# Kernel tuning notes

Measured on AMD Instinct MI355X. Metric: run time of the kernel, lower is better.

The kernel has to match this reference:

```python
import jax, jax.numpy as jnp
import numpy as np


def setup_inputs() -> dict:
    key = jax.random.key(0)
    ks = jax.random.split(key, 6)
    B, H, N, C, O, G = 4, 24, 512, 120, 512, 5
    x = jax.random.normal(ks[0], (B, H, N, C), dtype=jnp.float32)
    t_indices = jnp.arange(H, dtype=jnp.int64)
    time_emb = jax.random.normal(ks[1], (H, 8), dtype=jnp.float32)
    # kaiming-uniform-ish init for base linear weight
    fan_in = C + 8
    bound = float(np.sqrt(6.0 / fan_in))
    base_w = jax.random.uniform(ks[2], (O, C + 8), minval=-bound, maxval=bound, dtype=jnp.float32)
    base_b = jax.random.uniform(ks[3], (O,), minval=-1.0 / np.sqrt(fan_in), maxval=1.0 / np.sqrt(fan_in), dtype=jnp.float32)
    spline_weight = jax.random.uniform(ks[4], (O, C + 8, G), minval=-0.1, maxval=0.1, dtype=jnp.float32)
    return {"x": x, "t_indices": t_indices, "time_emb": time_emb,
            "base_w": base_w, "base_b": base_b, "spline_weight": spline_weight}


def reference(x, t_indices, time_emb, base_w, base_b, spline_weight):
    B, H, N, C = x.shape
    G = spline_weight.shape[-1]
    grid = jnp.linspace(-1.0, 1.0, G, dtype=x.dtype)  # non-trainable buffer
    # time embedding lookup, broadcast over batch and nodes: [B,H,N,8]
    t_emb = jnp.broadcast_to(time_emb[t_indices][None, :, None, :], (B, H, N, time_emb.shape[-1]))
    x_in = jnp.concatenate([x, t_emb], axis=-1)  # [B,H,N,C+8]
    # base path: SiLU then linear
    base = jnp.einsum('bhni,oi->bhno', jax.nn.silu(x_in), base_w) + base_b
    # RBF basis: [B,H,N,C+8,G]
    inv_h = (G - 1) / 2.0  # 1 / (2/(G-1))
    basis = jnp.exp(-(((x_in[..., None] - grid) * inv_h) ** 2))
    spline = jnp.einsum('bhnig,oig->bhno', basis, spline_weight)
    return base + spline
```

## Files before the change

kernel.cpp:

```cpp
#include <hip/hip_runtime.h>
#include <hip/hip_bf16.h>

typedef __attribute__((ext_vector_type(4))) float f32x4;
typedef __attribute__((ext_vector_type(8))) short bf16x8;

#define GLDS16(gp, lp) __builtin_amdgcn_global_load_lds( \
    (__attribute__((address_space(1))) void*)(void*)(gp), \
    (__attribute__((address_space(3))) void*)(lp), 16, 0, 0)

static constexpr int Mtot = 49152;
static constexpr int Otot = 512;
static constexpr int Hh   = 24;

__device__ inline unsigned short f2bf(float f) {
    __hip_bfloat16 h = __float2bfloat16(f);
    unsigned short u;
    __builtin_memcpy(&u, &h, 2);
    return u;
}

__global__ __launch_bounds__(256) void prep_W(
        const float* __restrict__ bw, const float* __restrict__ sw,
        uint4* __restrict__ Wt)
{
    const int tid = blockIdx.x * 256 + threadIdx.x;
    const int col = tid & 511;
    const int cc  = tid >> 9;
    const int k0  = cc * 8;
    unsigned short s[8];
    #pragma unroll
    for (int e = 0; e < 8; ++e) {
        const int k = k0 + e;
        const int i = k / 6, f = k - i * 6;
        const float v = (f == 0) ? bw[col * 128 + i]
                                 : sw[(col * 128 + i) * 5 + (f - 1)];
        s[e] = f2bf(v);
    }
    uint4 u;
    u.x = s[0] | ((unsigned)s[1] << 16);
    u.y = s[2] | ((unsigned)s[3] << 16);
    u.z = s[4] | ((unsigned)s[5] << 16);
    u.w = s[6] | ((unsigned)s[7] << 16);
    Wt[tid] = u;
}

__global__ __launch_bounds__(256, 3) void gemm_kan(
        const float* __restrict__ x, const int* __restrict__ t_idx,
        const float* __restrict__ temb,
        const char* __restrict__ Wt,
        const float* __restrict__ bias,
        float* __restrict__ out)
{
    __shared__ char Alds[12 * 128 * 16];
    __shared__ char Blds[12 * 128 * 16];
    const int t    = threadIdx.x;
    const int wave = t >> 6;
    const int lane = t & 63;
    const int ll   = lane & 15;
    const int q4   = lane >> 4;
    const int wm   = (wave >> 1) * 64;
    const int wn   = (wave & 1) * 64;

    const int bid = blockIdx.x;
    const int swz = (bid & 7) * 192 + (bid >> 3);
    const int m_base = (swz >> 2) * 128;
    const int n_base = (swz & 3) * 128;

    const int row = t >> 1;
    const int hh  = t & 1;
    const int ht  = t_idx[(m_base >> 9) % Hh];
    const float* xrow = x + (size_t)(m_base + row) * 120;
    const float* trow = temb + ht * 8;

    auto chanptr = [&](int i0) -> const float* {
        return (i0 < 120) ? (xrow + i0) : (trow + (i0 - 120));
    };

    f32x4 acc[4][4] = {};

    float4 xa, xb;
    {
        const float* p = chanptr(hh * 8);
        xa = *(const float4*)p;
        xb = *(const float4*)(p + 4);
    }

    constexpr float C1 = 0.36787944117f;
    constexpr float C4 = 0.01831563889f;

    #pragma unroll
    for (int it = 0; it < 8; ++it) {
        #pragma unroll
        for (int j = 0; j < 6; ++j) {
            const int c = wave * 3 + (j >> 1);
            const int g = (j & 1) * 64;
            const char* src = Wt + (((size_t)(it * 12 + c) * 512 + n_base + g) << 4)
                              + lane * 16;
            GLDS16(src, Blds + ((c * 128 + g) << 4));
        }

        const float4 ca = xa, cb = xb;
        if (it < 7) {
            const float* p = chanptr((it + 1) * 16 + hh * 8);
            xa = *(const float4*)p;
            xb = *(const float4*)(p + 4);
        }

        const float v[8] = {ca.x, ca.y, ca.z, ca.w, cb.x, cb.y, cb.z, cb.w};
        unsigned short s[48];
        #pragma unroll
        for (int c = 0; c < 8; ++c) {
            const float vv = v[c];
            s[c * 6 + 0] = f2bf(vv * __builtin_amdgcn_rcpf(1.0f + __expf(-vv)));
            const float tt = __expf(-4.0f * vv * vv);
            const float uu = __expf(4.0f * vv);
            const float rr = __builtin_amdgcn_rcpf(uu);
            const float tu = tt * uu, tr = tt * rr;
            s[c * 6 + 1] = f2bf(tr * rr * C4);
            s[c * 6 + 2] = f2bf(tr * C1);
            s[c * 6 + 3] = f2bf(tt);
            s[c * 6 + 4] = f2bf(tu * C1);
            s[c * 6 + 5] = f2bf(tu * uu * C4);
        }
        #pragma unroll
        for (int j = 0; j < 6; ++j) {
            const int ck = 6 * hh + j;
            unsigned u[4];
            #pragma unroll
            for (int n = 0; n < 4; ++n)
                u[n] = s[j * 8 + 2 * n] | ((unsigned)s[j * 8 + 2 * n + 1] << 16);
            *(uint4*)(Alds + ((ck * 128 + row) << 4)) = make_uint4(u[0], u[1], u[2], u[3]);
        }
        __syncthreads();

        #pragma unroll
        for (int kk = 0; kk < 3; ++kk) {
            const int ch = kk * 4 + q4;
            bf16x8 af[4], bf[4];
            #pragma unroll
            for (int mi = 0; mi < 4; ++mi)
                af[mi] = *(const bf16x8*)(Alds + ((ch * 128 + wm + mi * 16 + ll) << 4));
            #pragma unroll
            for (int ni = 0; ni < 4; ++ni)
                bf[ni] = *(const bf16x8*)(Blds + ((ch * 128 + wn + ni * 16 + ll) << 4));
            #pragma unroll
            for (int mi = 0; mi < 4; ++mi)
                #pragma unroll
                for (int ni = 0; ni < 4; ++ni)
                    acc[mi][ni] = __builtin_amdgcn_mfma_f32_16x16x32_bf16(
                        af[mi], bf[ni], acc[mi][ni], 0, 0, 0);
        }
        __syncthreads();
    }

    const int col0 = n_base + wn + ll;
    const int row0 = m_base + wm + q4 * 4;
    #pragma unroll
    for (int ni = 0; ni < 4; ++ni) {
        const int col = col0 + ni * 16;
        const float bv = bias[col];
        #pragma unroll
        for (int mi = 0; mi < 4; ++mi) {
            #pragma unroll
            for (int r = 0; r < 4; ++r) {
                out[(long)(row0 + mi * 16 + r) * Otot + col] = acc[mi][ni][r] + bv;
            }
        }
    }
}

extern "C" void kernel_launch(void* const* d_in, const int* in_sizes, int n_in,
                              void* d_out, int out_size, void* d_ws, size_t ws_size,
                              hipStream_t stream) {
    const float* x    = (const float*)d_in[0];
    const int*   tidx = (const int*)  d_in[1];
    const float* temb = (const float*)d_in[2];
    const float* bw   = (const float*)d_in[3];
    const float* bb   = (const float*)d_in[4];
    const float* sw   = (const float*)d_in[5];
    float* out = (float*)d_out;

    char* Wt = (char*)d_ws;

    prep_W<<<49152 / 256, 256, 0, stream>>>(bw, sw, (uint4*)Wt);
    gemm_kan<<<1536, 256, 0, stream>>>(x, tidx, temb, Wt, bb, out);
}
```

Before: 167.6 us.

## Retile GEMM to 96x256 blocks with six waves and fold RBF constants into weights

```diff
diff --git a/kernel.cpp b/kernel.cpp
--- a/kernel.cpp
+++ b/kernel.cpp
@@ -19,6 +19,9 @@
     return u;
 }
 
+static constexpr float C1 = 0.36787944117f;
+static constexpr float C4 = 0.01831563889f;
+
 __global__ __launch_bounds__(256) void prep_W(
         const float* __restrict__ bw, const float* __restrict__ sw,
         uint4* __restrict__ Wt)
@@ -27,13 +30,14 @@
     const int col = tid & 511;
     const int cc  = tid >> 9;
     const int k0  = cc * 8;
+    const float scale[6] = {1.0f, C4, C1, 1.0f, C1, C4};
     unsigned short s[8];
     #pragma unroll
     for (int e = 0; e < 8; ++e) {
         const int k = k0 + e;
         const int i = k / 6, f = k - i * 6;
         const float v = (f == 0) ? bw[col * 128 + i]
-                                 : sw[(col * 128 + i) * 5 + (f - 1)];
+                                 : sw[(col * 128 + i) * 5 + (f - 1)] * scale[f];
         s[e] = f2bf(v);
     }
     uint4 u;
@@ -44,31 +48,33 @@
     Wt[tid] = u;
 }
 
-__global__ __launch_bounds__(256, 3) void gemm_kan(
+static constexpr int APAD = 97;
+
+__global__ __launch_bounds__(384, 3) void gemm_kan(
         const float* __restrict__ x, const int* __restrict__ t_idx,
         const float* __restrict__ temb,
         const char* __restrict__ Wt,
         const float* __restrict__ bias,
         float* __restrict__ out)
 {
-    __shared__ char Alds[12 * 128 * 16];
-    __shared__ char Blds[12 * 128 * 16];
+    __shared__ char Alds[12 * APAD * 16];
+    __shared__ char Blds[12 * 256 * 16];
     const int t    = threadIdx.x;
     const int wave = t >> 6;
     const int lane = t & 63;
     const int ll   = lane & 15;
     const int q4   = lane >> 4;
-    const int wm   = (wave >> 1) * 64;
-    const int wn   = (wave & 1) * 64;
+    const int wm   = (wave >> 1) * 32;
+    const int wn   = (wave & 1) * 128;
 
     const int bid = blockIdx.x;
-    const int swz = (bid & 7) * 192 + (bid >> 3);
-    const int m_base = (swz >> 2) * 128;
-    const int n_base = (swz & 3) * 128;
+    const int swz = (bid & 7) * 128 + (bid >> 3);
+    const int m_base = (swz >> 1) * 96;
+    const int n_base = (swz & 1) * 256;
 
-    const int row = t >> 1;
-    const int hh  = t & 1;
-    const int ht  = t_idx[(m_base >> 9) % Hh];
+    const int row = t >> 2;
+    const int q   = t & 3;
+    const int ht  = t_idx[((m_base + row) >> 9) % Hh];
     const float* xrow = x + (size_t)(m_base + row) * 120;
     const float* trow = temb + ht * 8;
 
@@ -76,77 +82,65 @@
         return (i0 < 120) ? (xrow + i0) : (trow + (i0 - 120));
     };
 
-    f32x4 acc[4][4] = {};
+    f32x4 acc[2][8] = {};
 
-    float4 xa, xb;
-    {
-        const float* p = chanptr(hh * 8);
-        xa = *(const float4*)p;
-        xb = *(const float4*)(p + 4);
-    }
-
-    constexpr float C1 = 0.36787944117f;
-    constexpr float C4 = 0.01831563889f;
+    float4 xv = *(const float4*)chanptr(4 * q);
 
     #pragma unroll
     for (int it = 0; it < 8; ++it) {
         #pragma unroll
-        for (int j = 0; j < 6; ++j) {
-            const int c = wave * 3 + (j >> 1);
-            const int g = (j & 1) * 64;
-            const char* src = Wt + (((size_t)(it * 12 + c) * 512 + n_base + g) << 4)
-                              + lane * 16;
-            GLDS16(src, Blds + ((c * 128 + g) << 4));
+        for (int j = 0; j < 8; ++j) {
+            const int c = 2 * wave + (j >> 2);
+            const int g = (j & 3) * 64;
+            const char* src = Wt + (((size_t)(it * 12 + c) * 512 + n_base + g
+                                     + lane) << 4);
+            GLDS16(src, Blds + ((c * 256 + g) << 4));
         }
 
-        const float4 ca = xa, cb = xb;
-        if (it < 7) {
-            const float* p = chanptr((it + 1) * 16 + hh * 8);
-            xa = *(const float4*)p;
-            xb = *(const float4*)(p + 4);
-        }
+        const float4 cur = xv;
+        if (it < 7) xv = *(const float4*)chanptr((it + 1) * 16 + 4 * q);
 
-        const float v[8] = {ca.x, ca.y, ca.z, ca.w, cb.x, cb.y, cb.z, cb.w};
-        unsigned short s[48];
+        const float v[4] = {cur.x, cur.y, cur.z, cur.w};
+        unsigned short s[24];
         #pragma unroll
-        for (int c = 0; c < 8; ++c) {
+        for (int c = 0; c < 4; ++c) {
             const float vv = v[c];
             s[c * 6 + 0] = f2bf(vv * __builtin_amdgcn_rcpf(1.0f + __expf(-vv)));
             const float tt = __expf(-4.0f * vv * vv);
             const float uu = __expf(4.0f * vv);
             const float rr = __builtin_amdgcn_rcpf(uu);
             const float tu = tt * uu, tr = tt * rr;
-            s[c * 6 + 1] = f2bf(tr * rr * C4);
-            s[c * 6 + 2] = f2bf(tr * C1);
+            s[c * 6 + 1] = f2bf(tr * rr);
+            s[c * 6 + 2] = f2bf(tr);
             s[c * 6 + 3] = f2bf(tt);
-            s[c * 6 + 4] = f2bf(tu * C1);
-            s[c * 6 + 5] = f2bf(tu * uu * C4);
+            s[c * 6 + 4] = f2bf(tu);
+            s[c * 6 + 5] = f2bf(tu * uu);
         }
         #pragma unroll
-        for (int j = 0; j < 6; ++j) {
-            const int ck = 6 * hh + j;
+        for (int j = 0; j < 3; ++j) {
+            const int ck = 3 * q + j;
             unsigned u[4];
             #pragma unroll
             for (int n = 0; n < 4; ++n)
                 u[n] = s[j * 8 + 2 * n] | ((unsigned)s[j * 8 + 2 * n + 1] << 16);
-            *(uint4*)(Alds + ((ck * 128 + row) << 4)) = make_uint4(u[0], u[1], u[2], u[3]);
+            *(uint4*)(Alds + ((ck * APAD + row) << 4)) = make_uint4(u[0], u[1], u[2], u[3]);
         }
         __syncthreads();
 
         #pragma unroll
         for (int kk = 0; kk < 3; ++kk) {
             const int ch = kk * 4 + q4;
-            bf16x8 af[4], bf[4];
+            bf16x8 af[2], bf[8];
             #pragma unroll
-            for (int mi = 0; mi < 4; ++mi)
-                af[mi] = *(const bf16x8*)(Alds + ((ch * 128 + wm + mi * 16 + ll) << 4));
+            for (int mi = 0; mi < 2; ++mi)
+                af[mi] = *(const bf16x8*)(Alds + ((ch * APAD + wm + mi * 16 + ll) << 4));
             #pragma unroll
-            for (int ni = 0; ni < 4; ++ni)
-                bf[ni] = *(const bf16x8*)(Blds + ((ch * 128 + wn + ni * 16 + ll) << 4));
+            for (int ni = 0; ni < 8; ++ni)
+                bf[ni] = *(const bf16x8*)(Blds + ((ch * 256 + wn + ni * 16 + ll) << 4));
             #pragma unroll
-            for (int mi = 0; mi < 4; ++mi)
+            for (int mi = 0; mi < 2; ++mi)
                 #pragma unroll
-                for (int ni = 0; ni < 4; ++ni)
+                for (int ni = 0; ni < 8; ++ni)
                     acc[mi][ni] = __builtin_amdgcn_mfma_f32_16x16x32_bf16(
                         af[mi], bf[ni], acc[mi][ni], 0, 0, 0);
         }
@@ -156,11 +150,11 @@
     const int col0 = n_base + wn + ll;
     const int row0 = m_base + wm + q4 * 4;
     #pragma unroll
-    for (int ni = 0; ni < 4; ++ni) {
+    for (int ni = 0; ni < 8; ++ni) {
         const int col = col0 + ni * 16;
         const float bv = bias[col];
         #pragma unroll
-        for (int mi = 0; mi < 4; ++mi) {
+        for (int mi = 0; mi < 2; ++mi) {
             #pragma unroll
             for (int r = 0; r < 4; ++r) {
                 out[(long)(row0 + mi * 16 + r) * Otot + col] = acc[mi][ni][r] + bv;
@@ -183,5 +177,5 @@
     char* Wt = (char*)d_ws;
 
     prep_W<<<49152 / 256, 256, 0, stream>>>(bw, sw, (uint4*)Wt);
-    gemm_kan<<<1536, 256, 0, stream>>>(x, tidx, temb, Wt, bb, out);
+    gemm_kan<<<1024, 384, 0, stream>>>(x, tidx, temb, Wt, bb, out);
 }
```

Result: slower. 182.4 us (+8.9%).

## Precompute RBF/SiLU feature matrix in separate kernel and stream it into GEMM

Applied to the files above, without the earlier changes.

```diff
diff --git a/kernel.cpp b/kernel.cpp
--- a/kernel.cpp
+++ b/kernel.cpp
@@ -19,6 +19,9 @@
     return u;
 }
 
+static constexpr float C1 = 0.36787944117f;
+static constexpr float C4 = 0.01831563889f;
+
 __global__ __launch_bounds__(256) void prep_W(
         const float* __restrict__ bw, const float* __restrict__ sw,
         uint4* __restrict__ Wt)
@@ -27,13 +30,14 @@
     const int col = tid & 511;
     const int cc  = tid >> 9;
     const int k0  = cc * 8;
+    const float scale[6] = {1.0f, C4, C1, 1.0f, C1, C4};
     unsigned short s[8];
     #pragma unroll
     for (int e = 0; e < 8; ++e) {
         const int k = k0 + e;
         const int i = k / 6, f = k - i * 6;
         const float v = (f == 0) ? bw[col * 128 + i]
-                                 : sw[(col * 128 + i) * 5 + (f - 1)];
+                                 : sw[(col * 128 + i) * 5 + (f - 1)] * scale[f];
         s[e] = f2bf(v);
     }
     uint4 u;
@@ -44,9 +48,54 @@
     Wt[tid] = u;
 }
 
-__global__ __launch_bounds__(256, 3) void gemm_kan(
+__global__ __launch_bounds__(256) void featgen(
         const float* __restrict__ x, const int* __restrict__ t_idx,
         const float* __restrict__ temb,
+        uint4* __restrict__ Aimg)
+{
+    const int t    = threadIdx.x;
+    const int bid  = blockIdx.x;
+    const int lrow = t & 127;
+    const int grp  = ((bid & 7) << 1) | (t >> 7);
+    const int mt   = bid >> 3;
+    const int row  = mt * 128 + lrow;
+    const int ht   = t_idx[(row >> 9) % Hh];
+
+    const float* src = (grp < 15) ? (x + (size_t)row * 120 + grp * 8)
+                                  : (temb + ht * 8);
+    const float4 a = *(const float4*)src;
+    const float4 b = *(const float4*)(src + 4);
+    const float v[8] = {a.x, a.y, a.z, a.w, b.x, b.y, b.z, b.w};
+
+    unsigned short s[48];
+    #pragma unroll
+    for (int c = 0; c < 8; ++c) {
+        const float vv = v[c];
+        s[c * 6 + 0] = f2bf(vv * __builtin_amdgcn_rcpf(1.0f + __expf(-vv)));
+        const float tt = __expf(-4.0f * vv * vv);
+        const float uu = __expf(4.0f * vv);
+        const float rr = __builtin_amdgcn_rcpf(uu);
+        const float tu = tt * uu, tr = tt * rr;
+        s[c * 6 + 1] = f2bf(tr * rr);
+        s[c * 6 + 2] = f2bf(tr);
+        s[c * 6 + 3] = f2bf(tt);
+        s[c * 6 + 4] = f2bf(tu);
+        s[c * 6 + 5] = f2bf(tu * uu);
+    }
+
+    uint4* dst = Aimg + ((size_t)mt * 96 + grp * 6) * 128 + lrow;
+    #pragma unroll
+    for (int j = 0; j < 6; ++j) {
+        unsigned u[4];
+        #pragma unroll
+        for (int n = 0; n < 4; ++n)
+            u[n] = s[j * 8 + 2 * n] | ((unsigned)s[j * 8 + 2 * n + 1] << 16);
+        dst[j * 128] = make_uint4(u[0], u[1], u[2], u[3]);
+    }
+}
+
+__global__ __launch_bounds__(256, 3) void gemm_kan(
+        const char* __restrict__ Aimg,
         const char* __restrict__ Wt,
         const float* __restrict__ bias,
         float* __restrict__ out)
@@ -63,73 +112,29 @@
 
     const int bid = blockIdx.x;
     const int swz = (bid & 7) * 192 + (bid >> 3);
-    const int m_base = (swz >> 2) * 128;
+    const int mt  = swz >> 2;
+    const int m_base = mt * 128;
     const int n_base = (swz & 3) * 128;
 
-    const int row = t >> 1;
-    const int hh  = t & 1;
-    const int ht  = t_idx[(m_base >> 9) % Hh];
-    const float* xrow = x + (size_t)(m_base + row) * 120;
-    const float* trow = temb + ht * 8;
-
-    auto chanptr = [&](int i0) -> const float* {
-        return (i0 < 120) ? (xrow + i0) : (trow + (i0 - 120));
-    };
-
     f32x4 acc[4][4] = {};
-
-    float4 xa, xb;
-    {
-        const float* p = chanptr(hh * 8);
-        xa = *(const float4*)p;
-        xb = *(const float4*)(p + 4);
-    }
-
-    constexpr float C1 = 0.36787944117f;
-    constexpr float C4 = 0.01831563889f;
 
     #pragma unroll
     for (int it = 0; it < 8; ++it) {
         #pragma unroll
         for (int j = 0; j < 6; ++j) {
-            const int c = wave * 3 + (j >> 1);
-            const int g = (j & 1) * 64;
-            const char* src = Wt + (((size_t)(it * 12 + c) * 512 + n_base + g) << 4)
-                              + lane * 16;
-            GLDS16(src, Blds + ((c * 128 + g) << 4));
-        }
-
-        const float4 ca = xa, cb = xb;
-        if (it < 7) {
-            const float* p = chanptr((it + 1) * 16 + hh * 8);
-            xa = *(const float4*)p;
-            xb = *(const float4*)(p + 4);
-        }
-
-        const float v[8] = {ca.x, ca.y, ca.z, ca.w, cb.x, cb.y, cb.z, cb.w};
-        unsigned short s[48];
-        #pragma unroll
-        for (int c = 0; c < 8; ++c) {
-            const float vv = v[c];
-            s[c * 6 + 0] = f2bf(vv * __builtin_amdgcn_rcpf(1.0f + __expf(-vv)));
-            const float tt = __expf(-4.0f * vv * vv);
-            const float uu = __expf(4.0f * vv);
-            const float rr = __builtin_amdgcn_rcpf(uu);
-            const float tu = tt * uu, tr = tt * rr;
-            s[c * 6 + 1] = f2bf(tr * rr * C4);
-            s[c * 6 + 2] = f2bf(tr * C1);
-            s[c * 6 + 3] = f2bf(tt);
-            s[c * 6 + 4] = f2bf(tu * C1);
-            s[c * 6 + 5] = f2bf(tu * uu * C4);
+            const int c  = wave * 3 + (j >> 1);
+            const int rh = (j & 1) * 64;
+            const char* srcA = Aimg + (((size_t)mt * 96 + it * 12 + c) * 128
+                                       + rh + lane) * 16;
+            GLDS16(srcA, Alds + ((c * 128 + rh) << 4));
         }
         #pragma unroll
         for (int j = 0; j < 6; ++j) {
-            const int ck = 6 * hh + j;
-            unsigned u[4];
-            #pragma unroll
-            for (int n = 0; n < 4; ++n)
-                u[n] = s[j * 8 + 2 * n] | ((unsigned)s[j * 8 + 2 * n + 1] << 16);
-            *(uint4*)(Alds + ((ck * 128 + row) << 4)) = make_uint4(u[0], u[1], u[2], u[3]);
+            const int c = wave * 3 + (j >> 1);
+            const int g = (j & 1) * 64;
+            const char* srcB = Wt + (((size_t)(it * 12 + c) * 512 + n_base + g
+                                      + lane) << 4);
+            GLDS16(srcB, Blds + ((c * 128 + g) << 4));
         }
         __syncthreads();
 
@@ -180,8 +185,10 @@
     const float* sw   = (const float*)d_in[5];
     float* out = (float*)d_out;
 
-    char* Wt = (char*)d_ws;
+    char* Wt   = (char*)d_ws;
+    char* Aimg = (char*)d_ws + (1 << 20);
 
     prep_W<<<49152 / 256, 256, 0, stream>>>(bw, sw, (uint4*)Wt);
-    gemm_kan<<<1536, 256, 0, stream>>>(x, tidx, temb, Wt, bb, out);
+    featgen<<<3072, 256, 0, stream>>>(x, tidx, temb, (uint4*)Aimg);
+    gemm_kan<<<1536, 256, 0, stream>>>(Aimg, Wt, bb, out);
 }
```

Result: slower. 182.6 us (+9.0%).

## Double-buffer B tiles, overlap A generation with MFMA, fold RBF constants into weights

Applied to the files above, without the earlier changes.

```diff
diff --git a/kernel.cpp b/kernel.cpp
--- a/kernel.cpp
+++ b/kernel.cpp
@@ -18,6 +18,9 @@
     __builtin_memcpy(&u, &h, 2);
     return u;
 }
+
+static constexpr float C1 = 0.36787944117f;
+static constexpr float C4 = 0.01831563889f;
 
 __global__ __launch_bounds__(256) void prep_W(
         const float* __restrict__ bw, const float* __restrict__ sw,
@@ -27,13 +30,14 @@
     const int col = tid & 511;
     const int cc  = tid >> 9;
     const int k0  = cc * 8;
+    const float scale[6] = {1.0f, C4, C1, 1.0f, C1, C4};
     unsigned short s[8];
     #pragma unroll
     for (int e = 0; e < 8; ++e) {
         const int k = k0 + e;
         const int i = k / 6, f = k - i * 6;
         const float v = (f == 0) ? bw[col * 128 + i]
-                                 : sw[(col * 128 + i) * 5 + (f - 1)];
+                                 : sw[(col * 128 + i) * 5 + (f - 1)] * scale[f];
         s[e] = f2bf(v);
     }
     uint4 u;
@@ -44,7 +48,7 @@
     Wt[tid] = u;
 }
 
-__global__ __launch_bounds__(256, 3) void gemm_kan(
+__global__ __launch_bounds__(256, 2) void gemm_kan(
         const float* __restrict__ x, const int* __restrict__ t_idx,
         const float* __restrict__ temb,
         const char* __restrict__ Wt,
@@ -52,7 +56,7 @@
         float* __restrict__ out)
 {
     __shared__ char Alds[12 * 128 * 16];
-    __shared__ char Blds[12 * 128 * 16];
+    __shared__ char Blds[2][12 * 128 * 16];
     const int t    = threadIdx.x;
     const int wave = t >> 6;
     const int lane = t & 63;
@@ -76,36 +80,18 @@
         return (i0 < 120) ? (xrow + i0) : (trow + (i0 - 120));
     };
 
-    f32x4 acc[4][4] = {};
-
-    float4 xa, xb;
-    {
-        const float* p = chanptr(hh * 8);
-        xa = *(const float4*)p;
-        xb = *(const float4*)(p + 4);
-    }
-
-    constexpr float C1 = 0.36787944117f;
-    constexpr float C4 = 0.01831563889f;
-
-    #pragma unroll
-    for (int it = 0; it < 8; ++it) {
+    auto stageB = [&](int it, int buf) {
         #pragma unroll
         for (int j = 0; j < 6; ++j) {
             const int c = wave * 3 + (j >> 1);
             const int g = (j & 1) * 64;
-            const char* src = Wt + (((size_t)(it * 12 + c) * 512 + n_base + g) << 4)
-                              + lane * 16;
-            GLDS16(src, Blds + ((c * 128 + g) << 4));
-        }
-
-        const float4 ca = xa, cb = xb;
-        if (it < 7) {
-            const float* p = chanptr((it + 1) * 16 + hh * 8);
-            xa = *(const float4*)p;
-            xb = *(const float4*)(p + 4);
-        }
-
+            const char* src = Wt + (((size_t)(it * 12 + c) * 512 + n_base + g
+                                     + lane) << 4);
+            GLDS16(src, Blds[buf] + ((c * 128 + g) << 4));
+        }
+    };
+
+    auto gen = [&](const float4 ca, const float4 cb, uint4* au) {
         const float v[8] = {ca.x, ca.y, ca.z, ca.w, cb.x, cb.y, cb.z, cb.w};
         unsigned short s[48];
         #pragma unroll
@@ -116,23 +102,61 @@
             const float uu = __expf(4.0f * vv);
             const float rr = __builtin_amdgcn_rcpf(uu);
             const float tu = tt * uu, tr = tt * rr;
-            s[c * 6 + 1] = f2bf(tr * rr * C4);
-            s[c * 6 + 2] = f2bf(tr * C1);
+            s[c * 6 + 1] = f2bf(tr * rr);
+            s[c * 6 + 2] = f2bf(tr);
             s[c * 6 + 3] = f2bf(tt);
-            s[c * 6 + 4] = f2bf(tu * C1);
-            s[c * 6 + 5] = f2bf(tu * uu * C4);
-        }
+            s[c * 6 + 4] = f2bf(tu);
+            s[c * 6 + 5] = f2bf(tu * uu);
+        }
+        #pragma unroll
+        for (int j = 0; j < 6; ++j) {
+            unsigned u[4];
+            #pragma unroll
+            for (int n = 0; n < 4; ++n)
+                u[n] = s[j * 8 + 2 * n] | ((unsigned)s[j * 8 + 2 * n + 1] << 16);
+            au[j] = make_uint4(u[0], u[1], u[2], u[3]);
+        }
+    };
+
+    auto writeA = [&](const uint4* au) {
         #pragma unroll
         for (int j = 0; j < 6; ++j) {
             const int ck = 6 * hh + j;
-            unsigned u[4];
-            #pragma unroll
-            for (int n = 0; n < 4; ++n)
-                u[n] = s[j * 8 + 2 * n] | ((unsigned)s[j * 8 + 2 * n + 1] << 16);
-            *(uint4*)(Alds + ((ck * 128 + row) << 4)) = make_uint4(u[0], u[1], u[2], u[3]);
-        }
-        __syncthreads();
-
+            *(uint4*)(Alds + ((ck * 128 + row) << 4)) = au[j];
+        }
+    };
+
+    f32x4 acc[4][4] = {};
+
+    stageB(0, 0);
+    float4 pa, pb;
+    {
+        const float* p0 = chanptr(hh * 8);
+        const float4 xa = *(const float4*)p0;
+        const float4 xb = *(const float4*)(p0 + 4);
+        const float* p1 = chanptr(16 + hh * 8);
+        pa = *(const float4*)p1;
+        pb = *(const float4*)(p1 + 4);
+        uint4 a0[6];
+        gen(xa, xb, a0);
+        writeA(a0);
+    }
+    __syncthreads();
+
+    #pragma unroll
+    for (int it = 0; it < 8; ++it) {
+        if (it < 7) stageB(it + 1, (it + 1) & 1);
+
+        const float4 ca = pa, cb = pb;
+        if (it < 6) {
+            const float* p = chanptr((it + 2) * 16 + hh * 8);
+            pa = *(const float4*)p;
+            pb = *(const float4*)(p + 4);
+        }
+        uint4 au[6];
+        if (it < 7) gen(ca, cb, au);
+
+        const char* B = Blds[it & 1];
         #pragma unroll
         for (int kk = 0; kk < 3; ++kk) {
             const int ch = kk * 4 + q4;
@@ -142,7 +166,7 @@
                 af[mi] = *(const bf16x8*)(Alds + ((ch * 128 + wm + mi * 16 + ll) << 4));
             #pragma unroll
             for (int ni = 0; ni < 4; ++ni)
-                bf[ni] = *(const bf16x8*)(Blds + ((ch * 128 + wn + ni * 16 + ll) << 4));
+                bf[ni] = *(const bf16x8*)(B + ((ch * 128 + wn + ni * 16 + ll) << 4));
             #pragma unroll
             for (int mi = 0; mi < 4; ++mi)
                 #pragma unroll
@@ -150,7 +174,12 @@
                     acc[mi][ni] = __builtin_amdgcn_mfma_f32_16x16x32_bf16(
                         af[mi], bf[ni], acc[mi][ni], 0, 0, 0);
         }
-        __syncthreads();
+
+        if (it < 7) {
+            __syncthreads();
+            writeA(au);
+            __syncthreads();
+        }
     }
 
     const int col0 = n_base + wn + ll;
```

Measured after the change: 172.4 us. 2.9% more time.
